# Kernel optimization log

Measured on AMD Instinct MI355X. Metric: run time of the kernel, lower is better.

Reference implementation:

```python
import jax, jax.numpy as jnp
import numpy as np

D = 100  # hard-coded model dim from the source
L, BS = 4096, 64


def setup_inputs() -> dict:
    key = jax.random.key(0)
    k_x, k_w, k_b, k_s = jax.random.split(key, 4)
    x = jax.random.normal(k_x, (L, BS, 1, D), dtype=jnp.float32)
    # nn.Linear(D, D): weight [D, D] (out, in), bias [D]
    lim = 1.0 / np.sqrt(D)
    W = jax.random.uniform(k_w, (D, D), dtype=jnp.float32, minval=-lim, maxval=lim)
    b = jax.random.uniform(k_b, (D,), dtype=jnp.float32, minval=-lim, maxval=lim)
    # self.states ~ Normal(0, 0.02), shape [D, D]
    states = 0.02 * jax.random.normal(k_s, (D, D), dtype=jnp.float32)
    return {"x": x, "W": W, "b": b, "states": states}


def reference(x, W, b, states):
    # z1 = layer1(x): x [L, BS, 1, D] @ W.T + b
    z1 = jnp.einsum("lbod,ed->lboe", x, W) + b
    # scan: carry = tile(states) is constant across steps (f multiplies by 1.0),
    # so output[i] = z1[i] @ states for every timestep -> one fused batched matmul.
    out = jnp.einsum("lbod,de->lboe", z1, states)
    return out
```

## Files before the change

kernel.cpp:

```cpp
#include <hip/hip_runtime.h>

typedef __bf16 bf16x8 __attribute__((ext_vector_type(8)));
typedef float  f32x4  __attribute__((ext_vector_type(4)));

#define D100 100
#define NPAD 112
#define NROWS (4096*64)
#define NTILES (NROWS/16)
#define NCT 7
#define NKS 4
#define FRAG_ELEMS (NCT*NKS*64*8)
#define NBLK (NTILES/4)

__global__ __launch_bounds__(256) void prep_kernel(
    const float* __restrict__ W, const float* __restrict__ bvec,
    const float* __restrict__ S, __bf16* __restrict__ wsM,
    float* __restrict__ wsc) {
  int tid = blockIdx.x * 256 + threadIdx.x;
  if (tid < FRAG_ELEMS) {
    int j    = tid & 7;
    int lane = (tid >> 3) & 63;
    int ks   = (tid >> 9) & 3;
    int ct   = tid >> 11;
    int k = ks * 32 + ((lane >> 4) * 8) + j;
    int n = ct * 16 + (lane & 15);
    float acc = 0.f;
    if (k < D100 && n < D100) {
      float a0 = 0.f, a1 = 0.f, a2 = 0.f, a3 = 0.f;
      for (int d = 0; d < D100; d += 4) {
        a0 += W[(d + 0) * D100 + k] * S[(d + 0) * D100 + n];
        a1 += W[(d + 1) * D100 + k] * S[(d + 1) * D100 + n];
        a2 += W[(d + 2) * D100 + k] * S[(d + 2) * D100 + n];
        a3 += W[(d + 3) * D100 + k] * S[(d + 3) * D100 + n];
      }
      acc = (a0 + a1) + (a2 + a3);
    }
    wsM[tid] = (__bf16)acc;
  } else if (tid < FRAG_ELEMS + 128) {
    int n = tid - FRAG_ELEMS;
    if (n < NPAD) {
      float a = 0.f;
      if (n < D100)
        for (int d = 0; d < D100; ++d) a += bvec[d] * S[d * D100 + n];
      wsc[n] = a;
    }
  }
}

__global__ __launch_bounds__(256) void gemm_kernel(
    const float* __restrict__ x, const __bf16* __restrict__ wsM,
    const float* __restrict__ wsc, float* __restrict__ out) {
  __shared__ __align__(16) __bf16 ldsB[FRAG_ELEMS];

  const int t    = threadIdx.x;
  const int lane = t & 63;
  const int l16  = lane & 15;
  const int lg   = lane >> 4;
  const int tile = blockIdx.x * 4 + (t >> 6);

  {
    const f32x4* src = (const f32x4*)wsM;
    f32x4*       dst = (f32x4*)ldsB;
#pragma unroll
    for (int i = 0; i < 7; ++i) dst[i * 256 + t] = src[i * 256 + t];
  }

  const float* xr = x + (size_t)tile * (16 * D100) + l16 * D100;
  f32x4 xv[7];
#pragma unroll
  for (int ks = 0; ks < 3; ++ks) {
    xv[ks * 2]     = *(const f32x4*)(xr + ks * 32 + lg * 8);
    xv[ks * 2 + 1] = *(const f32x4*)(xr + ks * 32 + lg * 8 + 4);
  }
  xv[6] = (lg == 0) ? *(const f32x4*)(xr + 96) : (f32x4){0.f, 0.f, 0.f, 0.f};

  const f32x4* cv = (const f32x4*)wsc;
  f32x4 acc[NCT];
#pragma unroll
  for (int ct = 0; ct < NCT; ++ct) acc[ct] = cv[ct * 4 + lg];

  __syncthreads();

  const bf16x8* Bv = (const bf16x8*)ldsB;
#pragma unroll
  for (int ks = 0; ks < NKS; ++ks) {
    bf16x8 xf;
    if (ks < 3) {
      f32x4 v0 = xv[ks * 2], v1 = xv[ks * 2 + 1];
#pragma unroll
      for (int j = 0; j < 4; ++j) {
        xf[j]     = (__bf16)v0[j];
        xf[j + 4] = (__bf16)v1[j];
      }
    } else {
      f32x4 v0 = xv[6];
#pragma unroll
      for (int j = 0; j < 4; ++j) {
        xf[j]     = (__bf16)v0[j];
        xf[j + 4] = (__bf16)0.f;
      }
    }
#pragma unroll
    for (int ct = 0; ct < NCT; ++ct)
      acc[ct] = __builtin_amdgcn_mfma_f32_16x16x32_bf16(
          Bv[(ct * NKS + ks) * 64 + lane], xf, acc[ct], 0, 0, 0);
  }

  float* orow = out + (size_t)tile * (16 * D100) + l16 * D100 + lg * 4;
#pragma unroll
  for (int ct = 0; ct < NCT; ++ct) {
    if (ct < 6 || lg == 0)
      *(f32x4*)(orow + ct * 16) = acc[ct];
  }
}

extern "C" void kernel_launch(void* const* d_in, const int* in_sizes, int n_in,
                              void* d_out, int out_size, void* d_ws,
                              size_t ws_size, hipStream_t stream) {
  const float* x = (const float*)d_in[0];
  const float* W = (const float*)d_in[1];
  const float* b = (const float*)d_in[2];
  const float* S = (const float*)d_in[3];
  __bf16* wsM = (__bf16*)d_ws;
  float*  wsc = (float*)((char*)d_ws + (size_t)FRAG_ELEMS * 2);
  float*  out = (float*)d_out;

  hipLaunchKernelGGL(prep_kernel, dim3(57), dim3(256), 0, stream,
                     W, b, S, wsM, wsc);
  hipLaunchKernelGGL(gemm_kernel, dim3(NBLK), dim3(256), 0, stream,
                     x, wsM, wsc, out);
}
```

Before: 47.05 us.

## Persistent GEMM with double-buffered x loads and bias folded into MFMA

Replaces one-tile-per-wave blocks with a persistent grid of 1280 blocks. Each wave loops over tiles and prefetches the next tile's x into a second register set while computing the current one, so LDS staging of B is amortised and load latency overlaps compute. The bias term is folded into the padded K slot 112 of the weight fragment, with a constant 1.0 placed in the x fragment, which removes the separate bias vector and its accumulator init. Stores become nontemporal and launch bounds request 5 blocks per CU. The cost is higher register pressure from the double buffer and a serial per-wave loop.

```diff
diff --git a/kernel.cpp b/kernel.cpp
--- a/kernel.cpp
+++ b/kernel.cpp
@@ -4,28 +4,28 @@
 typedef float  f32x4  __attribute__((ext_vector_type(4)));
 
 #define D100 100
-#define NPAD 112
 #define NROWS (4096*64)
 #define NTILES (NROWS/16)
 #define NCT 7
 #define NKS 4
 #define FRAG_ELEMS (NCT*NKS*64*8)
-#define NBLK (NTILES/4)
+#define NBLK 1280
+#define WAVES (NBLK*4)
 
 __global__ __launch_bounds__(256) void prep_kernel(
     const float* __restrict__ W, const float* __restrict__ bvec,
-    const float* __restrict__ S, __bf16* __restrict__ wsM,
-    float* __restrict__ wsc) {
+    const float* __restrict__ S, __bf16* __restrict__ wsM) {
   int tid = blockIdx.x * 256 + threadIdx.x;
-  if (tid < FRAG_ELEMS) {
-    int j    = tid & 7;
-    int lane = (tid >> 3) & 63;
-    int ks   = (tid >> 9) & 3;
-    int ct   = tid >> 11;
-    int k = ks * 32 + ((lane >> 4) * 8) + j;
-    int n = ct * 16 + (lane & 15);
-    float acc = 0.f;
-    if (k < D100 && n < D100) {
+  if (tid >= FRAG_ELEMS) return;
+  int j    = tid & 7;
+  int lane = (tid >> 3) & 63;
+  int ks   = (tid >> 9) & 3;
+  int ct   = tid >> 11;
+  int k = ks * 32 + ((lane >> 4) * 8) + j;
+  int n = ct * 16 + (lane & 15);
+  float acc = 0.f;
+  if (n < D100) {
+    if (k < D100) {
       float a0 = 0.f, a1 = 0.f, a2 = 0.f, a3 = 0.f;
       for (int d = 0; d < D100; d += 4) {
         a0 += W[(d + 0) * D100 + k] * S[(d + 0) * D100 + n];
@@ -34,29 +34,23 @@
         a3 += W[(d + 3) * D100 + k] * S[(d + 3) * D100 + n];
       }
       acc = (a0 + a1) + (a2 + a3);
-    }
-    wsM[tid] = (__bf16)acc;
-  } else if (tid < FRAG_ELEMS + 128) {
-    int n = tid - FRAG_ELEMS;
-    if (n < NPAD) {
-      float a = 0.f;
-      if (n < D100)
-        for (int d = 0; d < D100; ++d) a += bvec[d] * S[d * D100 + n];
-      wsc[n] = a;
+    } else if (k == 112) {
+      for (int d = 0; d < D100; ++d) acc += bvec[d] * S[d * D100 + n];
     }
   }
+  wsM[tid] = (__bf16)acc;
 }
 
-__global__ __launch_bounds__(256) void gemm_kernel(
+__global__ __launch_bounds__(256, 5) void gemm_kernel(
     const float* __restrict__ x, const __bf16* __restrict__ wsM,
-    const float* __restrict__ wsc, float* __restrict__ out) {
+    float* __restrict__ out) {
   __shared__ __align__(16) __bf16 ldsB[FRAG_ELEMS];
 
   const int t    = threadIdx.x;
   const int lane = t & 63;
   const int l16  = lane & 15;
   const int lg   = lane >> 4;
-  const int tile = blockIdx.x * 4 + (t >> 6);
+  const int gwave = blockIdx.x * 4 + (t >> 6);
 
   {
     const f32x4* src = (const f32x4*)wsM;
@@ -65,52 +59,73 @@
     for (int i = 0; i < 7; ++i) dst[i * 256 + t] = src[i * 256 + t];
   }
 
-  const float* xr = x + (size_t)tile * (16 * D100) + l16 * D100;
-  f32x4 xv[7];
+  auto load_tile = [&](int tile, f32x4 (&xv)[7]) {
+    const float* xr = x + (size_t)tile * (16 * D100) + l16 * D100;
 #pragma unroll
-  for (int ks = 0; ks < 3; ++ks) {
-    xv[ks * 2]     = *(const f32x4*)(xr + ks * 32 + lg * 8);
-    xv[ks * 2 + 1] = *(const f32x4*)(xr + ks * 32 + lg * 8 + 4);
-  }
-  xv[6] = (lg == 0) ? *(const f32x4*)(xr + 96) : (f32x4){0.f, 0.f, 0.f, 0.f};
+    for (int ks = 0; ks < 3; ++ks) {
+      xv[ks * 2]     = *(const f32x4*)(xr + ks * 32 + lg * 8);
+      xv[ks * 2 + 1] = *(const f32x4*)(xr + ks * 32 + lg * 8 + 4);
+    }
+    xv[6] = (lg == 0) ? *(const f32x4*)(xr + 96) : (f32x4){0.f, 0.f, 0.f, 0.f};
+  };
 
-  const f32x4* cv = (const f32x4*)wsc;
-  f32x4 acc[NCT];
+  const bf16x8* Bv = (const bf16x8*)ldsB;
+
+  auto compute_store = [&](int tile, const f32x4 (&xv)[7]) {
+    f32x4 acc[NCT];
 #pragma unroll
-  for (int ct = 0; ct < NCT; ++ct) acc[ct] = cv[ct * 4 + lg];
+    for (int ct = 0; ct < NCT; ++ct) acc[ct] = (f32x4){0.f, 0.f, 0.f, 0.f};
 
+#pragma unroll
+    for (int ks = 0; ks < NKS; ++ks) {
+      bf16x8 xf;
+      if (ks < 3) {
+        f32x4 v0 = xv[ks * 2], v1 = xv[ks * 2 + 1];
+#pragma unroll
+        for (int j = 0; j < 4; ++j) {
+          xf[j]     = (__bf16)v0[j];
+          xf[j + 4] = (__bf16)v1[j];
+        }
+      } else {
+        f32x4 v0 = xv[6];
+#pragma unroll
+        for (int j = 0; j < 4; ++j) {
+          xf[j]     = (__bf16)v0[j];
+          xf[j + 4] = (__bf16)0.f;
+        }
+        if (lg == 2) xf[0] = (__bf16)1.0f;
+      }
+#pragma unroll
+      for (int ct = 0; ct < NCT; ++ct)
+        acc[ct] = __builtin_amdgcn_mfma_f32_16x16x32_bf16(
+            Bv[(ct * NKS + ks) * 64 + lane], xf, acc[ct], 0, 0, 0);
+    }
+
+    float* orow = out + (size_t)tile * (16 * D100) + l16 * D100 + lg * 4;
+#pragma unroll
+    for (int ct = 0; ct < NCT; ++ct) {
+      if (ct < 6 || lg == 0)
+        __builtin_nontemporal_store(acc[ct], (f32x4*)(orow + ct * 16));
+    }
+  };
+
+  f32x4 xva[7], xvb[7];
+  int tile = gwave;
+  load_tile(tile, xva);
   __syncthreads();
 
-  const bf16x8* Bv = (const bf16x8*)ldsB;
-#pragma unroll
-  for (int ks = 0; ks < NKS; ++ks) {
-    bf16x8 xf;
-    if (ks < 3) {
-      f32x4 v0 = xv[ks * 2], v1 = xv[ks * 2 + 1];
-#pragma unroll
-      for (int j = 0; j < 4; ++j) {
-        xf[j]     = (__bf16)v0[j];
-        xf[j + 4] = (__bf16)v1[j];
-      }
-    } else {
-      f32x4 v0 = xv[6];
-#pragma unroll
-      for (int j = 0; j < 4; ++j) {
-        xf[j]     = (__bf16)v0[j];
-        xf[j + 4] = (__bf16)0.f;
-      }
-    }
-#pragma unroll
-    for (int ct = 0; ct < NCT; ++ct)
-      acc[ct] = __builtin_amdgcn_mfma_f32_16x16x32_bf16(
-          Bv[(ct * NKS + ks) * 64 + lane], xf, acc[ct], 0, 0, 0);
-  }
+  for (;;) {
+    int n1 = tile + WAVES;
+    if (n1 < NTILES) load_tile(n1, xvb);
+    compute_store(tile, xva);
+    if (n1 >= NTILES) break;
 
-  float* orow = out + (size_t)tile * (16 * D100) + l16 * D100 + lg * 4;
-#pragma unroll
-  for (int ct = 0; ct < NCT; ++ct) {
-    if (ct < 6 || lg == 0)
-      *(f32x4*)(orow + ct * 16) = acc[ct];
+    tile = n1;
+    int n2 = tile + WAVES;
+    if (n2 < NTILES) load_tile(n2, xva);
+    compute_store(tile, xvb);
+    if (n2 >= NTILES) break;
+    tile = n2;
   }
 }
 
@@ -122,11 +137,10 @@
   const float* b = (const float*)d_in[2];
   const float* S = (const float*)d_in[3];
   __bf16* wsM = (__bf16*)d_ws;
-  float*  wsc = (float*)((char*)d_ws + (size_t)FRAG_ELEMS * 2);
   float*  out = (float*)d_out;
 
-  hipLaunchKernelGGL(prep_kernel, dim3(57), dim3(256), 0, stream,
-                     W, b, S, wsM, wsc);
+  hipLaunchKernelGGL(prep_kernel, dim3(56), dim3(256), 0, stream,
+                     W, b, S, wsM);
   hipLaunchKernelGGL(gemm_kernel, dim3(NBLK), dim3(256), 0, stream,
-                     x, wsM, wsc, out);
+                     x, wsM, out);
 }
```

Result: slower. 157.6 us (+235.0%).
